# Kernel optimization log

Measured on AMD Instinct MI355X. Metric: run time of the kernel, lower is better.

Reference implementation:

```python
import jax, jax.numpy as jnp
import numpy as np

D_IN = 1024
D_OUT = 1024
NUM_HEADS = 16
HEAD_DIM = D_OUT // NUM_HEADS
EPS = 1e-6
POW = 16.0


def setup_inputs() -> dict:
    key = jax.random.key(0)
    ks = jax.random.split(key, 6)
    s = 1.0 / np.sqrt(D_IN)
    x = jax.random.normal(ks[0], (2, 2048, D_IN), dtype=jnp.float32)
    Wq = jax.random.uniform(ks[1], (D_OUT, D_IN), jnp.float32, -s, s)
    Wk = jax.random.uniform(ks[2], (D_OUT, D_IN), jnp.float32, -s, s)
    Wv = jax.random.uniform(ks[3], (D_OUT, D_IN), jnp.float32, -s, s)
    Wo = jax.random.uniform(ks[4], (D_OUT, D_OUT), jnp.float32, -s, s)
    bo = jax.random.uniform(ks[5], (D_OUT,), jnp.float32, -s, s)
    return {"x": x, "Wq": Wq, "Wk": Wk, "Wv": Wv, "Wo": Wo, "bo": bo}


def _l2norm(t):
    # torch F.normalize: t / max(||t||, eps)
    n = jnp.sqrt(jnp.sum(t * t, axis=-1, keepdims=True))
    return t / jnp.maximum(n, EPS)


def reference(x, Wq, Wk, Wv, Wo, bo):
    B, T, _ = x.shape
    # project and split heads: [B, H, T, Dh]
    def heads(W):
        y = jnp.einsum('btd,od->bto', x, W)
        return y.reshape(B, T, NUM_HEADS, HEAD_DIM).transpose(0, 2, 1, 3)
    Q = _l2norm(heads(Wq))
    K = _l2norm(heads(Wk))
    V = heads(Wv)
    cos_sim = jnp.clip(jnp.einsum('bhtd,bhsd->bhts', Q, K), -0.999, 0.999)
    scores = 1.0 - jnp.arccos(cos_sim) / jnp.pi
    W = jnp.power(jnp.maximum(scores, EPS), POW)
    W = W / (jnp.sum(W, axis=-1, keepdims=True) + EPS)
    out = jnp.einsum('bhts,bhsd->bhtd', W, V)
    out = out.transpose(0, 2, 1, 3).reshape(B, T, D_OUT)
    return jnp.einsum('bto,po->btp', out, Wo) + bo
```

## Files before the change

kernel.cpp:

```cpp
#include <hip/hip_runtime.h>
#include <math.h>

constexpr int Dm   = 1024;
constexpr int NH   = 16;
constexpr int HD   = 64;
constexpr int Bb   = 2;
constexpr int Tt   = 2048;
constexpr int MTOT = Bb * Tt;
#define EPSF 1e-6f

typedef __attribute__((ext_vector_type(8))) short short8;
typedef __attribute__((ext_vector_type(4))) float f32x4;
typedef __attribute__((ext_vector_type(2))) float f32x2;

__device__ __forceinline__ ushort f2bf(float f) {
    union { float f; unsigned u; } v; v.f = f;
    unsigned r = (v.u + 0x7FFFu + ((v.u >> 16) & 1u)) >> 16;
    return (ushort)r;
}

__device__ __forceinline__ void gload16(const void* g, void* l) {
    __builtin_amdgcn_global_load_lds(
        (const __attribute__((address_space(1))) unsigned int*)g,
        (__attribute__((address_space(3))) unsigned int*)l,
        16, 0, 0);
}

__global__ __launch_bounds__(256)
void cvt_all(const float* __restrict__ x,  const float* __restrict__ wq,
             const float* __restrict__ wk, const float* __restrict__ wv,
             const float* __restrict__ wo,
             ushort* __restrict__ xb,  ushort* __restrict__ wqb,
             ushort* __restrict__ wkb, ushort* __restrict__ wvb,
             ushort* __restrict__ wob) {
    int i = blockIdx.x * 256 + threadIdx.x;
    const float* src; ushort* dst; int off;
    if (i < 1048576)      { src = x;  dst = xb;  off = i; }
    else if (i < 1310720) { src = wq; dst = wqb; off = i - 1048576; }
    else if (i < 1572864) { src = wk; dst = wkb; off = i - 1310720; }
    else if (i < 1835008) { src = wv; dst = wvb; off = i - 1572864; }
    else                  { src = wo; dst = wob; off = i - 1835008; }
    const float4 v = ((const float4*)src)[off];
    ushort4 o;
    o.x = f2bf(v.x); o.y = f2bf(v.y); o.z = f2bf(v.z); o.w = f2bf(v.w);
    ((ushort4*)dst)[off] = o;
}

template<bool OUTF32>
__device__ __forceinline__
void gemm_core(const ushort* __restrict__ A, const ushort* __restrict__ W,
               const float* __restrict__ bias, void* __restrict__ out,
               int m0, int n0, int N, int K, bool do_norm) {
    __shared__ ushort As[128 * 64];
    __shared__ ushort Bs[128 * 64];
    const int tid  = threadIdx.x;
    const int wave = tid >> 6, lane = tid & 63;
    const int quad = lane >> 4, l15 = lane & 15;
    const int wr = wave >> 1, wc = wave & 1;
    const int lr = lane >> 3;
    const int sc = (lane & 7) ^ lr;

    f32x4 acc[4][4] = {};
    const ushort* Ab = A + (size_t)(m0 + lr) * K + sc * 8;
    const ushort* Wb = W + (size_t)(n0 + lr) * K + sc * 8;

    for (int k0 = 0; k0 < K; k0 += 64) {
        #pragma unroll
        for (int i = 0; i < 4; i++) {
            const int rows8 = (wave * 4 + i) * 8;
            gload16(Ab + (size_t)rows8 * K + k0, &As[rows8 * 64]);
            gload16(Wb + (size_t)rows8 * K + k0, &Bs[rows8 * 64]);
        }
        __syncthreads();
        #pragma unroll
        for (int kh = 0; kh < 2; kh++) {
            short8 af[4];
            #pragma unroll
            for (int mi = 0; mi < 4; mi++) {
                const int row = wr * 64 + mi * 16 + l15;
                af[mi] = *(const short8*)&As[row * 64 + (((kh * 4 + quad) ^ (row & 7)) * 8)];
            }
            #pragma unroll
            for (int nj = 0; nj < 4; nj++) {
                const int row = wc * 64 + nj * 16 + l15;
                const short8 bf = *(const short8*)&Bs[row * 64 + (((kh * 4 + quad) ^ (row & 7)) * 8)];
                #pragma unroll
                for (int mi = 0; mi < 4; mi++)
                    acc[mi][nj] = __builtin_amdgcn_mfma_f32_16x16x32_bf16(af[mi], bf, acc[mi][nj], 0, 0, 0);
            }
        }
        __syncthreads();
    }

    #pragma unroll
    for (int mi = 0; mi < 4; mi++) {
        float inv[4] = {1.f, 1.f, 1.f, 1.f};
        if (!OUTF32 && do_norm) {
            #pragma unroll
            for (int r = 0; r < 4; r++) {
                float ss = 0.f;
                #pragma unroll
                for (int nj = 0; nj < 4; nj++) ss += acc[mi][nj][r] * acc[mi][nj][r];
                ss += __shfl_xor(ss, 1); ss += __shfl_xor(ss, 2);
                ss += __shfl_xor(ss, 4); ss += __shfl_xor(ss, 8);
                inv[r] = 1.f / fmaxf(sqrtf(ss), EPSF);
            }
        }
        #pragma unroll
        for (int nj = 0; nj < 4; nj++)
            #pragma unroll
            for (int r = 0; r < 4; r++) {
                const int row = m0 + wr * 64 + mi * 16 + quad * 4 + r;
                const int col = n0 + wc * 64 + nj * 16 + l15;
                if (OUTF32)
                    ((float*)out)[(size_t)row * N + col] = acc[mi][nj][r] + bias[col];
                else
                    ((ushort*)out)[(size_t)row * N + col] = f2bf(acc[mi][nj][r] * inv[r]);
            }
    }
}

__global__ __launch_bounds__(256)
void qkv_gemm(const ushort* __restrict__ xb,
              const ushort* __restrict__ wq, const ushort* __restrict__ wk,
              const ushort* __restrict__ wv,
              ushort* __restrict__ qb, ushort* __restrict__ kb,
              ushort* __restrict__ vb) {
    const int ny = blockIdx.y, sel = ny >> 3;
    const ushort* W = (sel == 0) ? wq : (sel == 1) ? wk : wv;
    ushort* out     = (sel == 0) ? qb : (sel == 1) ? kb : vb;
    gemm_core<false>(xb, W, nullptr, out, blockIdx.x * 128, (ny & 7) * 128,
                     Dm, Dm, sel < 2);
}

__global__ __launch_bounds__(256)
void out_gemm(const ushort* __restrict__ aob, const ushort* __restrict__ wob,
              const float* __restrict__ bias, float* __restrict__ out) {
    gemm_core<true>(aob, wob, bias, out, blockIdx.x * 128, blockIdx.y * 128,
                    Dm, Dm, false);
}

__global__ __launch_bounds__(256)
void vtranspose(const ushort* __restrict__ vb, ushort* __restrict__ vtb) {
    __shared__ ushort T[64][72];
    const int tid = threadIdx.x;
    const int s0 = blockIdx.x * 64, h = blockIdx.y, b = blockIdx.z;
    const size_t vtbase = (size_t)((b * NH + h) * HD) * Tt;
    for (int c = tid; c < 512; c += 256) {
        const int s = c >> 3, d0 = (c & 7) * 8;
        *(short8*)&T[s][d0] =
            *(const short8*)&vb[(size_t)(b * Tt + s0 + s) * Dm + h * HD + d0];
    }
    __syncthreads();
    for (int c = tid; c < 512; c += 256) {
        const int d = c >> 3, scol = (c & 7) * 8;
        short8 val;
        #pragma unroll
        for (int i = 0; i < 8; i++) val[i] = (short)T[scol + i][d];
        *(short8*)&vtb[vtbase + (size_t)d * Tt + s0 + scol] = val;
    }
}

__global__ __launch_bounds__(256)
void attn_kernel(const ushort* __restrict__ Qb, const ushort* __restrict__ Kb,
                 const ushort* __restrict__ Vtb, ushort* __restrict__ Ob) {
    __shared__ ushort Ks[64][72];
    __shared__ ushort Vs[64][72];
    __shared__ ushort Ws[64][72];
    const int tid  = threadIdx.x;
    const int wave = tid >> 6, lane = tid & 63;
    const int quad = lane >> 4, l15 = lane & 15;
    const int t0 = blockIdx.x * 64, h = blockIdx.y, b = blockIdx.z;

    const size_t qrow = (size_t)(b * Tt + t0 + 16 * wave + l15) * Dm + h * HD;
    const short8 qf0 = *(const short8*)&Qb[qrow + quad * 8];
    const short8 qf1 = *(const short8*)&Qb[qrow + 32 + quad * 8];

    f32x4 oacc[4] = {};
    float den[4] = {0.f, 0.f, 0.f, 0.f};
    const size_t kbase  = (size_t)(b * Tt) * Dm + h * HD;
    const size_t vtbase = (size_t)((b * NH + h) * HD) * Tt;

    const f32x2 k3 = {-0.00596162f, -0.00596162f};
    const f32x2 k2 = { 0.02363680f,  0.02363680f};
    const f32x2 k1 = {-0.06751768f, -0.06751768f};
    const f32x2 k0 = { 0.49997415f,  0.49997415f};

    for (int s0 = 0; s0 < Tt; s0 += 64) {
        for (int c = tid; c < 512; c += 256) {
            const int r = c >> 3, cc = (c & 7) * 8;
            *(short8*)&Ks[r][cc] = *(const short8*)&Kb[kbase + (size_t)(s0 + r) * Dm + cc];
            *(short8*)&Vs[r][cc] = *(const short8*)&Vtb[vtbase + (size_t)r * Tt + s0 + cc];
        }
        __syncthreads();

        f32x4 sf[4] = {};
        #pragma unroll
        for (int j = 0; j < 4; j++) {
            const short8 kf0 = *(const short8*)&Ks[16 * j + l15][quad * 8];
            const short8 kf1 = *(const short8*)&Ks[16 * j + l15][32 + quad * 8];
            sf[j] = __builtin_amdgcn_mfma_f32_16x16x32_bf16(qf0, kf0, sf[j], 0, 0, 0);
            sf[j] = __builtin_amdgcn_mfma_f32_16x16x32_bf16(qf1, kf1, sf[j], 0, 0, 0);
        }

        #pragma unroll
        for (int r = 0; r < 4; r++) {
            f32x2 ca, cb;
            ca.x = __builtin_amdgcn_fmed3f(sf[0][r], -0.999f, 0.999f);
            ca.y = __builtin_amdgcn_fmed3f(sf[1][r], -0.999f, 0.999f);
            cb.x = __builtin_amdgcn_fmed3f(sf[2][r], -0.999f, 0.999f);
            cb.y = __builtin_amdgcn_fmed3f(sf[3][r], -0.999f, 0.999f);
            f32x2 axa = {fabsf(ca.x), fabsf(ca.y)};
            f32x2 axb = {fabsf(cb.x), fabsf(cb.y)};
            f32x2 pa = __builtin_elementwise_fma(axa, k3, k2);
            f32x2 pb = __builtin_elementwise_fma(axb, k3, k2);
            pa = __builtin_elementwise_fma(pa, axa, k1);
            pb = __builtin_elementwise_fma(pb, axb, k1);
            pa = __builtin_elementwise_fma(pa, axa, k0);
            pb = __builtin_elementwise_fma(pb, axb, k0);
            f32x2 ta = 1.0f - axa, tb = 1.0f - axb;
            ta.x = __builtin_amdgcn_sqrtf(ta.x); ta.y = __builtin_amdgcn_sqrtf(ta.y);
            tb.x = __builtin_amdgcn_sqrtf(tb.x); tb.y = __builtin_amdgcn_sqrtf(tb.y);
            const f32x2 rpa = ta * pa, rpb = tb * pb;
            const f32x2 da = 0.5f - rpa, db = 0.5f - rpb;
            f32x2 csa = {__builtin_copysignf(da.x, ca.x), __builtin_copysignf(da.y, ca.y)};
            f32x2 csb = {__builtin_copysignf(db.x, cb.x), __builtin_copysignf(db.y, cb.y)};
            f32x2 wa = csa + 0.5f, wb = csb + 0.5f;
            wa *= wa; wa *= wa; wa *= wa; wa *= wa;
            wb *= wb; wb *= wb; wb *= wb; wb *= wb;
            den[r] += (wa.x + wa.y) + (wb.x + wb.y);
            const int wrow = 16 * wave + quad * 4 + r;
            Ws[wrow][l15]      = f2bf(wa.x);
            Ws[wrow][16 + l15] = f2bf(wa.y);
            Ws[wrow][32 + l15] = f2bf(wb.x);
            Ws[wrow][48 + l15] = f2bf(wb.y);
        }
        __syncthreads();

        const short8 wf0 = *(const short8*)&Ws[16 * wave + l15][quad * 8];
        const short8 wf1 = *(const short8*)&Ws[16 * wave + l15][32 + quad * 8];
        #pragma unroll
        for (int j = 0; j < 4; j++) {
            const short8 vf0 = *(const short8*)&Vs[16 * j + l15][quad * 8];
            const short8 vf1 = *(const short8*)&Vs[16 * j + l15][32 + quad * 8];
            oacc[j] = __builtin_amdgcn_mfma_f32_16x16x32_bf16(wf0, vf0, oacc[j], 0, 0, 0);
            oacc[j] = __builtin_amdgcn_mfma_f32_16x16x32_bf16(wf1, vf1, oacc[j], 0, 0, 0);
        }
        __syncthreads();
    }

    #pragma unroll
    for (int r = 0; r < 4; r++) {
        float d = den[r];
        d += __shfl_xor(d, 1); d += __shfl_xor(d, 2);
        d += __shfl_xor(d, 4); d += __shfl_xor(d, 8);
        den[r] = d;
    }
    const size_t obase = (size_t)(b * Tt + t0 + 16 * wave + quad * 4) * Dm + h * HD + l15;
    #pragma unroll
    for (int j = 0; j < 4; j++)
        #pragma unroll
        for (int r = 0; r < 4; r++)
            Ob[obase + (size_t)r * Dm + 16 * j] = f2bf(oacc[j][r] / (den[r] + EPSF));
}

extern "C" void kernel_launch(void* const* d_in, const int* in_sizes, int n_in,
                              void* d_out, int out_size, void* d_ws, size_t ws_size,
                              hipStream_t stream) {
    const float* x  = (const float*)d_in[0];
    const float* Wq = (const float*)d_in[1];
    const float* Wk = (const float*)d_in[2];
    const float* Wv = (const float*)d_in[3];
    const float* Wo = (const float*)d_in[4];
    const float* bo = (const float*)d_in[5];
    float* out = (float*)d_out;

    ushort* ws = (ushort*)d_ws;
    const size_t M1 = 1u << 20;
    ushort* xb  = ws;
    ushort* wqb = ws + 4 * M1;
    ushort* wkb = ws + 5 * M1;
    ushort* wvb = ws + 6 * M1;
    ushort* wob = ws + 7 * M1;
    ushort* qb  = ws + 8 * M1;
    ushort* kb  = ws + 12 * M1;
    ushort* vb  = ws + 16 * M1;
    ushort* vtb = ws + 20 * M1;
    ushort* aob = ws + 24 * M1;

    cvt_all<<<8192, 256, 0, stream>>>(x, Wq, Wk, Wv, Wo, xb, wqb, wkb, wvb, wob);
    qkv_gemm<<<dim3(MTOT / 128, 24), 256, 0, stream>>>(xb, wqb, wkb, wvb, qb, kb, vb);
    vtranspose<<<dim3(Tt / 64, NH, Bb), 256, 0, stream>>>(vb, vtb);
    attn_kernel<<<dim3(Tt / 64, NH, Bb), 256, 0, stream>>>(qb, kb, vtb, aob);
    out_gemm<<<dim3(MTOT / 128, Dm / 128), 256, 0, stream>>>(aob, wob, bo, out);
}
```

Before: 250.1 us.

## Double-buffer K/V tiles, use 128-query blocks, and XOR-swizzle LDS in attention

The attention kernel now handles 128 query rows per block, with each wave owning two 16-row MFMA tiles, so every K/V tile loaded into LDS is reused twice as often. The next K/V tile is prefetched into registers during compute and written to a second LDS buffer, which removes one barrier per iteration and hides global-load latency. LDS padding is replaced by an XOR swizzle to avoid bank conflicts. In exchange the grid shrinks to 512 blocks and register pressure rises, which may lower occupancy.

```diff
diff --git a/kernel.cpp b/kernel.cpp
--- a/kernel.cpp
+++ b/kernel.cpp
@@ -164,104 +164,153 @@
 __global__ __launch_bounds__(256)
 void attn_kernel(const ushort* __restrict__ Qb, const ushort* __restrict__ Kb,
                  const ushort* __restrict__ Vtb, ushort* __restrict__ Ob) {
-    __shared__ ushort Ks[64][72];
-    __shared__ ushort Vs[64][72];
-    __shared__ ushort Ws[64][72];
+    __shared__ ushort Ks[2][64 * 64];
+    __shared__ ushort Vs[2][64 * 64];
+    __shared__ ushort Ws[128 * 64];
     const int tid  = threadIdx.x;
     const int wave = tid >> 6, lane = tid & 63;
     const int quad = lane >> 4, l15 = lane & 15;
-    const int t0 = blockIdx.x * 64, h = blockIdx.y, b = blockIdx.z;
-
-    const size_t qrow = (size_t)(b * Tt + t0 + 16 * wave + l15) * Dm + h * HD;
-    const short8 qf0 = *(const short8*)&Qb[qrow + quad * 8];
-    const short8 qf1 = *(const short8*)&Qb[qrow + 32 + quad * 8];
-
-    f32x4 oacc[4] = {};
-    float den[4] = {0.f, 0.f, 0.f, 0.f};
+    const int t0 = blockIdx.x * 128, h = blockIdx.y, b = blockIdx.z;
+
+    short8 qf[2][2];
+    #pragma unroll
+    for (int mi = 0; mi < 2; mi++) {
+        const size_t qrow =
+            (size_t)(b * Tt + t0 + 32 * wave + 16 * mi + l15) * Dm + h * HD;
+        qf[mi][0] = *(const short8*)&Qb[qrow + quad * 8];
+        qf[mi][1] = *(const short8*)&Qb[qrow + 32 + quad * 8];
+    }
+
     const size_t kbase  = (size_t)(b * Tt) * Dm + h * HD;
     const size_t vtbase = (size_t)((b * NH + h) * HD) * Tt;
+    const int r0 = tid >> 3, ch0 = tid & 7;
+    const ushort* kg = Kb  + kbase  + (size_t)r0 * Dm + ch0 * 8;
+    const ushort* vg = Vtb + vtbase + (size_t)r0 * Tt + ch0 * 8;
+    const int lsw0 = r0 * 64 + ((ch0 ^ (r0 & 7)) * 8);
+    const int lsw1 = (r0 + 32) * 64 + ((ch0 ^ (r0 & 7)) * 8);
+
+    f32x4 oacc[2][4] = {};
+    f32x2 denp[2][4] = {};
 
     const f32x2 k3 = {-0.00596162f, -0.00596162f};
     const f32x2 k2 = { 0.02363680f,  0.02363680f};
     const f32x2 k1 = {-0.06751768f, -0.06751768f};
     const f32x2 k0 = { 0.49997415f,  0.49997415f};
 
-    for (int s0 = 0; s0 < Tt; s0 += 64) {
-        for (int c = tid; c < 512; c += 256) {
-            const int r = c >> 3, cc = (c & 7) * 8;
-            *(short8*)&Ks[r][cc] = *(const short8*)&Kb[kbase + (size_t)(s0 + r) * Dm + cc];
-            *(short8*)&Vs[r][cc] = *(const short8*)&Vtb[vtbase + (size_t)r * Tt + s0 + cc];
-        }
+    short8 pk0 = *(const short8*)kg;
+    short8 pk1 = *(const short8*)(kg + (size_t)32 * Dm);
+    short8 pv0 = *(const short8*)vg;
+    short8 pv1 = *(const short8*)(vg + (size_t)32 * Tt);
+    *(short8*)&Ks[0][lsw0] = pk0;  *(short8*)&Ks[0][lsw1] = pk1;
+    *(short8*)&Vs[0][lsw0] = pv0;  *(short8*)&Vs[0][lsw1] = pv1;
+    __syncthreads();
+
+    for (int i = 0; i < 32; i++) {
+        const int p = i & 1;
+        if (i < 31) {
+            const size_t sn = (size_t)(i + 1) * 64;
+            pk0 = *(const short8*)(kg + sn * Dm);
+            pk1 = *(const short8*)(kg + (sn + 32) * Dm);
+            pv0 = *(const short8*)(vg + sn);
+            pv1 = *(const short8*)(vg + sn + (size_t)32 * Tt);
+        }
+
+        f32x4 sf[2][4] = {};
+        #pragma unroll
+        for (int j = 0; j < 4; j++) {
+            const int row = 16 * j + l15;
+            const short8 kf0 = *(const short8*)&Ks[p][row * 64 + ((quad ^ (row & 7)) * 8)];
+            const short8 kf1 = *(const short8*)&Ks[p][row * 64 + (((4 + quad) ^ (row & 7)) * 8)];
+            #pragma unroll
+            for (int mi = 0; mi < 2; mi++) {
+                sf[mi][j] = __builtin_amdgcn_mfma_f32_16x16x32_bf16(qf[mi][0], kf0, sf[mi][j], 0, 0, 0);
+                sf[mi][j] = __builtin_amdgcn_mfma_f32_16x16x32_bf16(qf[mi][1], kf1, sf[mi][j], 0, 0, 0);
+            }
+        }
+
+        #pragma unroll
+        for (int mi = 0; mi < 2; mi++)
+            #pragma unroll
+            for (int r = 0; r < 4; r++) {
+                f32x2 ca, cb;
+                ca.x = __builtin_amdgcn_fmed3f(sf[mi][0][r], -0.999f, 0.999f);
+                ca.y = __builtin_amdgcn_fmed3f(sf[mi][1][r], -0.999f, 0.999f);
+                cb.x = __builtin_amdgcn_fmed3f(sf[mi][2][r], -0.999f, 0.999f);
+                cb.y = __builtin_amdgcn_fmed3f(sf[mi][3][r], -0.999f, 0.999f);
+                f32x2 axa = {fabsf(ca.x), fabsf(ca.y)};
+                f32x2 axb = {fabsf(cb.x), fabsf(cb.y)};
+                f32x2 pa = __builtin_elementwise_fma(axa, k3, k2);
+                f32x2 pb = __builtin_elementwise_fma(axb, k3, k2);
+                pa = __builtin_elementwise_fma(pa, axa, k1);
+                pb = __builtin_elementwise_fma(pb, axb, k1);
+                pa = __builtin_elementwise_fma(pa, axa, k0);
+                pb = __builtin_elementwise_fma(pb, axb, k0);
+                f32x2 ta = 1.0f - axa, tb = 1.0f - axb;
+                ta.x = __builtin_amdgcn_sqrtf(ta.x); ta.y = __builtin_amdgcn_sqrtf(ta.y);
+                tb.x = __builtin_amdgcn_sqrtf(tb.x); tb.y = __builtin_amdgcn_sqrtf(tb.y);
+                const f32x2 rpa = ta * pa, rpb = tb * pb;
+                const f32x2 da = 0.5f - rpa, db = 0.5f - rpb;
+                f32x2 csa = {__builtin_copysignf(da.x, ca.x), __builtin_copysignf(da.y, ca.y)};
+                f32x2 csb = {__builtin_copysignf(db.x, cb.x), __builtin_copysignf(db.y, cb.y)};
+                f32x2 wa = csa + 0.5f, wb = csb + 0.5f;
+                wa *= wa; wa *= wa; wa *= wa; wa *= wa;
+                wb *= wb; wb *= wb; wb *= wb; wb *= wb;
+                denp[mi][r] += wa; denp[mi][r] += wb;
+                const int wrow = 32 * wave + 16 * mi + quad * 4 + r;
+                const int wb7 = wrow & 7;
+                const int base = wrow * 64 + (l15 & 7);
+                const int hc = l15 >> 3;
+                Ws[base + (((hc)     ^ wb7) * 8)] = f2bf(wa.x);
+                Ws[base + (((hc + 2) ^ wb7) * 8)] = f2bf(wa.y);
+                Ws[base + (((hc + 4) ^ wb7) * 8)] = f2bf(wb.x);
+                Ws[base + (((hc + 6) ^ wb7) * 8)] = f2bf(wb.y);
+            }
         __syncthreads();
 
-        f32x4 sf[4] = {};
+        short8 wf[2][2];
+        #pragma unroll
+        for (int mi = 0; mi < 2; mi++) {
+            const int wrow = 32 * wave + 16 * mi + l15;
+            wf[mi][0] = *(const short8*)&Ws[wrow * 64 + ((quad ^ (wrow & 7)) * 8)];
+            wf[mi][1] = *(const short8*)&Ws[wrow * 64 + (((4 + quad) ^ (wrow & 7)) * 8)];
+        }
         #pragma unroll
         for (int j = 0; j < 4; j++) {
-            const short8 kf0 = *(const short8*)&Ks[16 * j + l15][quad * 8];
-            const short8 kf1 = *(const short8*)&Ks[16 * j + l15][32 + quad * 8];
-            sf[j] = __builtin_amdgcn_mfma_f32_16x16x32_bf16(qf0, kf0, sf[j], 0, 0, 0);
-            sf[j] = __builtin_amdgcn_mfma_f32_16x16x32_bf16(qf1, kf1, sf[j], 0, 0, 0);
-        }
-
+            const int vrow = 16 * j + l15;
+            const short8 vf0 = *(const short8*)&Vs[p][vrow * 64 + ((quad ^ (vrow & 7)) * 8)];
+            const short8 vf1 = *(const short8*)&Vs[p][vrow * 64 + (((4 + quad) ^ (vrow & 7)) * 8)];
+            #pragma unroll
+            for (int mi = 0; mi < 2; mi++) {
+                oacc[mi][j] = __builtin_amdgcn_mfma_f32_16x16x32_bf16(wf[mi][0], vf0, oacc[mi][j], 0, 0, 0);
+                oacc[mi][j] = __builtin_amdgcn_mfma_f32_16x16x32_bf16(wf[mi][1], vf1, oacc[mi][j], 0, 0, 0);
+            }
+        }
+        if (i < 31) {
+            *(short8*)&Ks[1 - p][lsw0] = pk0;  *(short8*)&Ks[1 - p][lsw1] = pk1;
+            *(short8*)&Vs[1 - p][lsw0] = pv0;  *(short8*)&Vs[1 - p][lsw1] = pv1;
+        }
+        __syncthreads();
+    }
+
+    #pragma unroll
+    for (int mi = 0; mi < 2; mi++) {
+        float den[4];
         #pragma unroll
         for (int r = 0; r < 4; r++) {
-            f32x2 ca, cb;
-            ca.x = __builtin_amdgcn_fmed3f(sf[0][r], -0.999f, 0.999f);
-            ca.y = __builtin_amdgcn_fmed3f(sf[1][r], -0.999f, 0.999f);
-            cb.x = __builtin_amdgcn_fmed3f(sf[2][r], -0.999f, 0.999f);
-            cb.y = __builtin_amdgcn_fmed3f(sf[3][r], -0.999f, 0.999f);
-            f32x2 axa = {fabsf(ca.x), fabsf(ca.y)};
-            f32x2 axb = {fabsf(cb.x), fabsf(cb.y)};
-            f32x2 pa = __builtin_elementwise_fma(axa, k3, k2);
-            f32x2 pb = __builtin_elementwise_fma(axb, k3, k2);
-            pa = __builtin_elementwise_fma(pa, axa, k1);
-            pb = __builtin_elementwise_fma(pb, axb, k1);
-            pa = __builtin_elementwise_fma(pa, axa, k0);
-            pb = __builtin_elementwise_fma(pb, axb, k0);
-            f32x2 ta = 1.0f - axa, tb = 1.0f - axb;
-            ta.x = __builtin_amdgcn_sqrtf(ta.x); ta.y = __builtin_amdgcn_sqrtf(ta.y);
-            tb.x = __builtin_amdgcn_sqrtf(tb.x); tb.y = __builtin_amdgcn_sqrtf(tb.y);
-            const f32x2 rpa = ta * pa, rpb = tb * pb;
-            const f32x2 da = 0.5f - rpa, db = 0.5f - rpb;
-            f32x2 csa = {__builtin_copysignf(da.x, ca.x), __builtin_copysignf(da.y, ca.y)};
-            f32x2 csb = {__builtin_copysignf(db.x, cb.x), __builtin_copysignf(db.y, cb.y)};
-            f32x2 wa = csa + 0.5f, wb = csb + 0.5f;
-            wa *= wa; wa *= wa; wa *= wa; wa *= wa;
-            wb *= wb; wb *= wb; wb *= wb; wb *= wb;
-            den[r] += (wa.x + wa.y) + (wb.x + wb.y);
-            const int wrow = 16 * wave + quad * 4 + r;
-            Ws[wrow][l15]      = f2bf(wa.x);
-            Ws[wrow][16 + l15] = f2bf(wa.y);
-            Ws[wrow][32 + l15] = f2bf(wb.x);
-            Ws[wrow][48 + l15] = f2bf(wb.y);
-        }
-        __syncthreads();
-
-        const short8 wf0 = *(const short8*)&Ws[16 * wave + l15][quad * 8];
-        const short8 wf1 = *(const short8*)&Ws[16 * wave + l15][32 + quad * 8];
-        #pragma unroll
-        for (int j = 0; j < 4; j++) {
-            const short8 vf0 = *(const short8*)&Vs[16 * j + l15][quad * 8];
-            const short8 vf1 = *(const short8*)&Vs[16 * j + l15][32 + quad * 8];
-            oacc[j] = __builtin_amdgcn_mfma_f32_16x16x32_bf16(wf0, vf0, oacc[j], 0, 0, 0);
-            oacc[j] = __builtin_amdgcn_mfma_f32_16x16x32_bf16(wf1, vf1, oacc[j], 0, 0, 0);
-        }
-        __syncthreads();
-    }
-
-    #pragma unroll
-    for (int r = 0; r < 4; r++) {
-        float d = den[r];
-        d += __shfl_xor(d, 1); d += __shfl_xor(d, 2);
-        d += __shfl_xor(d, 4); d += __shfl_xor(d, 8);
-        den[r] = d;
-    }
-    const size_t obase = (size_t)(b * Tt + t0 + 16 * wave + quad * 4) * Dm + h * HD + l15;
-    #pragma unroll
-    for (int j = 0; j < 4; j++)
-        #pragma unroll
-        for (int r = 0; r < 4; r++)
-            Ob[obase + (size_t)r * Dm + 16 * j] = f2bf(oacc[j][r] / (den[r] + EPSF));
+            float d = denp[mi][r].x + denp[mi][r].y;
+            d += __shfl_xor(d, 1); d += __shfl_xor(d, 2);
+            d += __shfl_xor(d, 4); d += __shfl_xor(d, 8);
+            den[r] = d;
+        }
+        const size_t obase =
+            (size_t)(b * Tt + t0 + 32 * wave + 16 * mi + quad * 4) * Dm + h * HD + l15;
+        #pragma unroll
+        for (int j = 0; j < 4; j++)
+            #pragma unroll
+            for (int r = 0; r < 4; r++)
+                Ob[obase + (size_t)r * Dm + 16 * j] =
+                    f2bf(oacc[mi][j][r] / (den[r] + EPSF));
+    }
 }
 
 extern "C" void kernel_launch(void* const* d_in, const int* in_sizes, int n_in,
@@ -291,6 +340,6 @@
     cvt_all<<<8192, 256, 0, stream>>>(x, Wq, Wk, Wv, Wo, xb, wqb, wkb, wvb, wob);
     qkv_gemm<<<dim3(MTOT / 128, 24), 256, 0, stream>>>(xb, wqb, wkb, wvb, qb, kb, vb);
     vtranspose<<<dim3(Tt / 64, NH, Bb), 256, 0, stream>>>(vb, vtb);
-    attn_kernel<<<dim3(Tt / 64, NH, Bb), 256, 0, stream>>>(qb, kb, vtb, aob);
+    attn_kernel<<<dim3(Tt / 128, NH, Bb), 256, 0, stream>>>(qb, kb, vtb, aob);
     out_gemm<<<dim3(MTOT / 128, Dm / 128), 256, 0, stream>>>(aob, wob, bo, out);
 }
```

New measurement: 242.4 us. 1.03x faster.
